# Optimization experiments

Hardware: AMD Instinct MI355X
Metric: run time of the kernel (lower is better)

Reference implementation:

```python
import jax, jax.numpy as jnp
import numpy as np

T, B, N, D = 32, 16, 2048, 64  # time steps, batch, nodes, dr2


def setup_inputs() -> dict:
    key = jax.random.key(0)
    k1, k2, k3, k4 = jax.random.split(key, 4)
    all_data_static = jax.random.normal(k1, (T, B, N, D), dtype=jnp.float32)
    thre_nc = jax.random.uniform(k2, (T, B, N, 1), dtype=jnp.float32)
    all_data_dynamic_now = jax.random.normal(k3, (B, N, D), dtype=jnp.float32)
    w1 = jax.random.normal(k4, (2 * D, D), dtype=jnp.float32) * 0.02
    return {
        "all_data_static": all_data_static,
        "thre_nc": thre_nc,
        "all_data_dynamic_now": all_data_dynamic_now,
        "w1": w1,
    }


def reference(all_data_static, thre_nc, all_data_dynamic_now, w1):
    # Sequential gated recurrent update over time steps 1..T-1.
    def step(h, xs):
        s, t = xs  # s: [B,N,D] static feat, t: [B,N,1] gate
        z = jnp.matmul(jnp.concatenate([h, s], axis=-1), w1)  # [B,N,D]
        h_new = jax.nn.sigmoid(z * t + h * (1.0 - t))
        return h_new, (h_new, h_new - h)

    _, (hs, diffs) = jax.lax.scan(
        step, all_data_dynamic_now, (all_data_static[1:], thre_nc[1:])
    )
    all_dyn = jnp.concatenate([all_data_dynamic_now[None], hs], axis=0)  # [T,B,N,D]
    final = hs[-1]  # [B,N,D]
    return all_dyn, final, diffs  # diffs: [T-1,B,N,D]
```

## Files before the change

kernel.cpp:

```cpp
#include <hip/hip_runtime.h>

constexpr int T = 32;
constexpr int NROWS = 16 * 2048;
constexpr int D = 64;
constexpr long DYN = (long)T * NROWS * D;
constexpr long FIN = (long)NROWS * D;

typedef float f32x4  __attribute__((ext_vector_type(4)));
typedef short bf16x8 __attribute__((ext_vector_type(8)));

__device__ __forceinline__ short f2b(float f) {
    union { float f; unsigned u; } v; v.f = f;
    unsigned r = (v.u + 0x7fffu + ((v.u >> 16) & 1u)) >> 16;
    return (short)r;
}


__global__ __launch_bounds__(128) void evo_kernel(
    const float* __restrict__ stat,
    const float* __restrict__ thre,
    const float* __restrict__ h0,
    const float* __restrict__ w1,
    float* __restrict__ out)
{
    __shared__ float hbuf[16 * 64];
    __shared__ float zS[16][68];
    __shared__ float zH[16][68];

    const int lane = threadIdx.x & 63;
    const int wv   = __builtin_amdgcn_readfirstlane(threadIdx.x >> 6);
    const int row0 = blockIdx.x * 16;
    const int m = lane & 15;
    const int q = lane >> 4;

    auto hptr = [&](int row, int col) -> float* {
        int byte = ((row * 64 + col) * 4) ^ ((row & 7) << 4);
        return (float*)((char*)hbuf + byte);
    };
    auto hquad = [&](int row, int c0) -> f32x4 {
        int byte = ((row * 64 + c0) * 4) ^ ((row & 7) << 4);
        return *(const f32x4*)((const char*)hbuf + byte);
    };

    bf16x8 B[2][4];
    {
        const float* wb = w1 + (long)(wv * 64) * 64;
#pragma unroll
        for (int kc = 0; kc < 2; ++kc)
#pragma unroll
            for (int g = 0; g < 4; ++g) {
                bf16x8 t;
#pragma unroll
                for (int j = 0; j < 8; ++j)
                    t[j] = f2b(wb[(kc * 32 + q * 8 + j) * 64 + m + 16 * g]);
                B[kc][g] = t;
            }
    }

#pragma unroll
    for (int i2 = 0; i2 < 8; ++i2) {
        int i = wv * 8 + i2;
        float hv = h0[(long)(row0 + i) * D + lane];
        __builtin_nontemporal_store(hv, out + (long)(row0 + i) * D + lane);
        *hptr(i, lane) = hv;
    }

    f32x4 sf[4];
    if (wv == 1) {
        const float* sp = stat + ((long)1 * NROWS + row0) * D;
#pragma unroll
        for (int kc = 0; kc < 2; ++kc)
#pragma unroll
            for (int hh = 0; hh < 2; ++hh)
                sf[kc * 2 + hh] = __builtin_nontemporal_load(
                    (const f32x4*)(sp + m * 64 + kc * 32 + q * 8 + hh * 4));
    }
    __syncthreads();

#pragma unroll 1
    for (int tt = 1; tt < T; ++tt) {
        bf16x8 A[2];
        if (wv == 0) {
#pragma unroll
            for (int kc = 0; kc < 2; ++kc) {
                f32x4 lo = hquad(m, kc * 32 + q * 8);
                f32x4 hi = hquad(m, kc * 32 + q * 8 + 4);
                bf16x8 a;
#pragma unroll
                for (int e = 0; e < 4; ++e) { a[e] = f2b(lo[e]); a[4 + e] = f2b(hi[e]); }
                A[kc] = a;
            }
        } else {
#pragma unroll
            for (int kc = 0; kc < 2; ++kc) {
                bf16x8 a;
#pragma unroll
                for (int e = 0; e < 4; ++e) { a[e] = f2b(sf[kc * 2][e]); a[4 + e] = f2b(sf[kc * 2 + 1][e]); }
                A[kc] = a;
            }
        }

        f32x4 dacc[4] = {{0.f,0.f,0.f,0.f},{0.f,0.f,0.f,0.f},{0.f,0.f,0.f,0.f},{0.f,0.f,0.f,0.f}};
#pragma unroll
        for (int g = 0; g < 4; ++g)
#pragma unroll
            for (int kc = 0; kc < 2; ++kc)
                dacc[g] = __builtin_amdgcn_mfma_f32_16x16x32_bf16(A[kc], B[kc][g], dacc[g], 0, 0, 0);

        float (*zbuf)[68] = wv ? zS : zH;
#pragma unroll
        for (int g = 0; g < 4; ++g)
#pragma unroll
            for (int rr = 0; rr < 4; ++rr)
                zbuf[q * 4 + rr][m + 16 * g] = dacc[g][rr];

        if (wv == 1 && tt + 1 < T) {
            const float* sp = stat + ((long)(tt + 1) * NROWS + row0) * D;
#pragma unroll
            for (int kc = 0; kc < 2; ++kc)
#pragma unroll
                for (int hh = 0; hh < 2; ++hh)
                    sf[kc * 2 + hh] = __builtin_nontemporal_load(
                        (const f32x4*)(sp + m * 64 + kc * 32 + q * 8 + hh * 4));
        }

        __syncthreads();

        {
            const float* tp = thre + (long)tt * NROWS + row0;
            float* od = out + ((long)tt * NROWS + row0) * D + lane;
            float* dd = out + DYN + FIN + ((long)(tt - 1) * NROWS + row0) * D + lane;
#pragma unroll
            for (int i2 = 0; i2 < 8; ++i2) {
                int i  = wv * 8 + i2;
                float z  = zS[i][lane] + zH[i][lane];
                float hp = *hptr(i, lane);
                float tg = tp[i];
                float v  = fmaf(tg, z - hp, hp);
                float hn = 1.0f / (1.0f + __expf(-v));
                float df = hn - hp;
                *hptr(i, lane) = hn;
                __builtin_nontemporal_store(hn, od + (long)i * D);
                __builtin_nontemporal_store(df, dd + (long)i * D);
                if (tt == T - 1)
                    __builtin_nontemporal_store(hn, out + DYN + (long)(row0 + i) * D + lane);
            }
        }
        __syncthreads();
    }
}

extern "C" void kernel_launch(void* const* d_in, const int* in_sizes, int n_in,
                              void* d_out, int out_size, void* d_ws, size_t ws_size,
                              hipStream_t stream) {
    const float* stat = (const float*)d_in[0];
    const float* thre = (const float*)d_in[1];
    const float* h0   = (const float*)d_in[2];
    const float* w1   = (const float*)d_in[3];
    float* out = (float*)d_out;

    dim3 grid(NROWS / 16);
    dim3 block(128);
    evo_kernel<<<grid, block, 0, stream>>>(stat, thre, h0, w1, out);
}
```

Before: 155.6 us.

## Keep recurrent state in bf16 shared memory and prefetch inputs a step ahead

The hidden state in shared memory is now stored as bf16 instead of swizzled fp32. The MMA A-operand can then be read directly without per-step conversion, and the elementwise update reads the previous state as bf16. The gate values and next-step static features are loaded at the top of each step into a double buffer, so their latency overlaps the matmul. The cost is that the previous state used in the gate blend and in the diff output is bf16-rounded, so error can compound across time steps.

```diff
diff --git a/kernel.cpp b/kernel.cpp
--- a/kernel.cpp
+++ b/kernel.cpp
@@ -14,6 +14,10 @@
     unsigned r = (v.u + 0x7fffu + ((v.u >> 16) & 1u)) >> 16;
     return (short)r;
 }
+__device__ __forceinline__ float b2f(short b) {
+    union { float f; unsigned u; } v; v.u = ((unsigned)(unsigned short)b) << 16;
+    return v.f;
+}
 
 
 __global__ __launch_bounds__(128) void evo_kernel(
@@ -23,7 +27,7 @@
     const float* __restrict__ w1,
     float* __restrict__ out)
 {
-    __shared__ float hbuf[16 * 64];
+    __shared__ short hb16[16][64];
     __shared__ float zS[16][68];
     __shared__ float zH[16][68];
 
@@ -32,15 +36,6 @@
     const int row0 = blockIdx.x * 16;
     const int m = lane & 15;
     const int q = lane >> 4;
-
-    auto hptr = [&](int row, int col) -> float* {
-        int byte = ((row * 64 + col) * 4) ^ ((row & 7) << 4);
-        return (float*)((char*)hbuf + byte);
-    };
-    auto hquad = [&](int row, int c0) -> f32x4 {
-        int byte = ((row * 64 + c0) * 4) ^ ((row & 7) << 4);
-        return *(const f32x4*)((const char*)hbuf + byte);
-    };
 
     bf16x8 B[2][4];
     {
@@ -62,40 +57,49 @@
         int i = wv * 8 + i2;
         float hv = h0[(long)(row0 + i) * D + lane];
         __builtin_nontemporal_store(hv, out + (long)(row0 + i) * D + lane);
-        *hptr(i, lane) = hv;
+        hb16[i][lane] = f2b(hv);
     }
 
-    f32x4 sf[4];
+    f32x4 sfA[4], sfB[4];
     if (wv == 1) {
         const float* sp = stat + ((long)1 * NROWS + row0) * D;
 #pragma unroll
         for (int kc = 0; kc < 2; ++kc)
 #pragma unroll
             for (int hh = 0; hh < 2; ++hh)
-                sf[kc * 2 + hh] = __builtin_nontemporal_load(
+                sfA[kc * 2 + hh] = __builtin_nontemporal_load(
                     (const f32x4*)(sp + m * 64 + kc * 32 + q * 8 + hh * 4));
     }
     __syncthreads();
 
 #pragma unroll 1
     for (int tt = 1; tt < T; ++tt) {
+        const float* tp = thre + (long)tt * NROWS + row0 + wv * 8;
+        float tg8[8];
+#pragma unroll
+        for (int i2 = 0; i2 < 8; ++i2) tg8[i2] = tp[i2];
+
+        if (wv == 1 && tt + 1 < T) {
+            const float* sp = stat + ((long)(tt + 1) * NROWS + row0) * D;
+#pragma unroll
+            for (int kc = 0; kc < 2; ++kc)
+#pragma unroll
+                for (int hh = 0; hh < 2; ++hh)
+                    sfB[kc * 2 + hh] = __builtin_nontemporal_load(
+                        (const f32x4*)(sp + m * 64 + kc * 32 + q * 8 + hh * 4));
+        }
+
         bf16x8 A[2];
         if (wv == 0) {
 #pragma unroll
-            for (int kc = 0; kc < 2; ++kc) {
-                f32x4 lo = hquad(m, kc * 32 + q * 8);
-                f32x4 hi = hquad(m, kc * 32 + q * 8 + 4);
-                bf16x8 a;
-#pragma unroll
-                for (int e = 0; e < 4; ++e) { a[e] = f2b(lo[e]); a[4 + e] = f2b(hi[e]); }
-                A[kc] = a;
-            }
+            for (int kc = 0; kc < 2; ++kc)
+                A[kc] = *(const bf16x8*)&hb16[m][kc * 32 + q * 8];
         } else {
 #pragma unroll
             for (int kc = 0; kc < 2; ++kc) {
                 bf16x8 a;
 #pragma unroll
-                for (int e = 0; e < 4; ++e) { a[e] = f2b(sf[kc * 2][e]); a[4 + e] = f2b(sf[kc * 2 + 1][e]); }
+                for (int e = 0; e < 4; ++e) { a[e] = f2b(sfA[kc * 2][e]); a[4 + e] = f2b(sfA[kc * 2 + 1][e]); }
                 A[kc] = a;
             }
         }
@@ -114,32 +118,20 @@
             for (int rr = 0; rr < 4; ++rr)
                 zbuf[q * 4 + rr][m + 16 * g] = dacc[g][rr];
 
-        if (wv == 1 && tt + 1 < T) {
-            const float* sp = stat + ((long)(tt + 1) * NROWS + row0) * D;
-#pragma unroll
-            for (int kc = 0; kc < 2; ++kc)
-#pragma unroll
-                for (int hh = 0; hh < 2; ++hh)
-                    sf[kc * 2 + hh] = __builtin_nontemporal_load(
-                        (const f32x4*)(sp + m * 64 + kc * 32 + q * 8 + hh * 4));
-        }
-
         __syncthreads();
 
         {
-            const float* tp = thre + (long)tt * NROWS + row0;
             float* od = out + ((long)tt * NROWS + row0) * D + lane;
             float* dd = out + DYN + FIN + ((long)(tt - 1) * NROWS + row0) * D + lane;
 #pragma unroll
             for (int i2 = 0; i2 < 8; ++i2) {
                 int i  = wv * 8 + i2;
                 float z  = zS[i][lane] + zH[i][lane];
-                float hp = *hptr(i, lane);
-                float tg = tp[i];
-                float v  = fmaf(tg, z - hp, hp);
+                float hp = b2f(hb16[i][lane]);
+                float v  = fmaf(tg8[i2], z - hp, hp);
                 float hn = 1.0f / (1.0f + __expf(-v));
                 float df = hn - hp;
-                *hptr(i, lane) = hn;
+                hb16[i][lane] = f2b(hn);
                 __builtin_nontemporal_store(hn, od + (long)i * D);
                 __builtin_nontemporal_store(df, dd + (long)i * D);
                 if (tt == T - 1)
@@ -147,6 +139,11 @@
             }
         }
         __syncthreads();
+
+        if (wv == 1 && tt + 1 < T) {
+#pragma unroll
+            for (int c = 0; c < 4; ++c) sfA[c] = sfB[c];
+        }
     }
 }
 
```

Measured after the change: 156.8 us. About the same (+0.8%).
